# Performance work log

Hardware: AMD Instinct MI355X
Metric: run time of the kernel (lower is better)

The kernel has to match this reference:

```python
import jax, jax.numpy as jnp
import numpy as np

B, S = 4, 512
D_IN, D_H = 1600, 1600
HEADS = 50
PH = D_H // HEADS  # 32, per-head size
N_REL = 100


def setup_inputs() -> dict:
    key = jax.random.key(0)
    ks = jax.random.split(key, 14)
    w = lambda k, shape: (jax.random.normal(k, shape, jnp.float32) * 0.02)
    return {
        "hidden": jax.random.normal(ks[0], (B, S, D_IN), jnp.float32),
        "Wq": w(ks[1], (D_IN, D_H)), "bq": jnp.zeros((D_H,), jnp.float32),
        "Wk": w(ks[2], (D_IN, D_H)), "bk": jnp.zeros((D_H,), jnp.float32),
        "Wv": w(ks[3], (D_IN, D_H)), "bv": jnp.zeros((D_H,), jnp.float32),
        "Wo": w(ks[4], (D_H, D_H)), "bo": jnp.zeros((D_H,), jnp.float32),
        "rel_k_emb": w(ks[5], (N_REL, PH)),
        "rel_v_emb": w(ks[6], (N_REL, PH)),
        "W1": w(ks[7], (D_H, D_H)), "b1": jnp.zeros((D_H,), jnp.float32),
        "W2": w(ks[8], (D_H, D_H)), "b2": jnp.zeros((D_H,), jnp.float32),
        "relationship_matrix": jax.random.randint(ks[9], (B, S, S), 0, N_REL),
    }


def reference(hidden, Wq, bq, Wk, bk, Wv, bv, Wo, bo,
              rel_k_emb, rel_v_emb, W1, b1, W2, b2, relationship_matrix):
    b, s, _ = hidden.shape

    def split_heads(x):  # [b,s,D_H] -> [b,h,s,ph]
        return x.reshape(b, s, HEADS, PH).transpose(0, 2, 1, 3)

    q = split_heads(hidden @ Wq + bq)
    k = split_heads(hidden @ Wk + bk)
    v = split_heads(hidden @ Wv + bv)

    # relation-aware bias: gather per-(query,key) relation embeddings
    rel_k = rel_k_emb[relationship_matrix]  # [b,s,s,ph]
    rel_v = rel_v_emb[relationship_matrix]  # [b,s,s,ph]

    scores = jnp.einsum('bhqd,bhkd->bhqk', q, k) \
           + jnp.einsum('bhqd,bqkd->bhqk', q, rel_k)
    probs = jax.nn.softmax(scores / np.float32(np.sqrt(PH)), axis=-1)

    ctx = jnp.einsum('bhqk,bhkd->bhqd', probs, v) \
        + jnp.einsum('bhqk,bqkd->bhqd', probs, rel_v)
    ctx = ctx.transpose(0, 2, 1, 3).reshape(b, s, D_H)
    attn_out = ctx @ Wo + bo

    # position-wise FFN (hidden -> hidden -> hidden), exact gelu
    h = jax.nn.gelu(attn_out @ W1 + b1, approximate=False)
    return h @ W2 + b2
```

## Files before the change

### kernel.cpp

```cpp
#include <hip/hip_runtime.h>
#include <math.h>

#define B_   4
#define S_   512
#define DH   1600
#define NH   50
#define PH   32
#define NREL 100
#define MROWS (B_ * S_)

typedef _Float16 f16x8 __attribute__((ext_vector_type(8)));
typedef float  floatx4 __attribute__((ext_vector_type(4)));

__device__ __forceinline__ float gelu_f(float x) {
    return 0.5f * x * (1.0f + erff(x * 0.70710678118654752f));
}

__device__ __forceinline__ unsigned short f2h_u(float f) {
    _Float16 h = (_Float16)f;
    return __builtin_bit_cast(unsigned short, h);
}

typedef const __attribute__((address_space(1))) unsigned int guint;
typedef __attribute__((address_space(3))) unsigned int luint;
__device__ __forceinline__ void gl_lds16(const unsigned short* g, unsigned short* l)
{
    __builtin_amdgcn_global_load_lds((guint*)g, (luint*)l, 16, 0, 0);
}

__device__ __forceinline__ void xcd_swizzle(int& bx, int& by)
{
    const int nx = gridDim.x, nwg = nx * gridDim.y;
    const int lin = blockIdx.y * nx + blockIdx.x;
    const int cpx = nwg >> 3;
    const int swz = (lin & 7) * cpx + (lin >> 3);
    bx = swz % nx; by = swz / nx;
}

__global__ __launch_bounds__(256)
void fcast_k(const float* __restrict__ in, unsigned short* __restrict__ out, int n4)
{
    int i = blockIdx.x * 256 + threadIdx.x;
    if (i < n4) {
        float4 v = *(const float4*)&in[i * 4];
        ushort4 o = { f2h_u(v.x), f2h_u(v.y), f2h_u(v.z), f2h_u(v.w) };
        *(ushort4*)&out[i * 4] = o;
    }
}

__global__ __launch_bounds__(256)
void wcast_k(const float* __restrict__ W0, const float* __restrict__ W1,
             const float* __restrict__ W2, const float* __restrict__ W3,
             const float* __restrict__ W4, const float* __restrict__ W5,
             unsigned short* __restrict__ T)
{
    const int z = blockIdx.z;
    const float* W = (z==0)?W0:(z==1)?W1:(z==2)?W2:(z==3)?W3:(z==4)?W4:W5;
    unsigned short* out = T + (size_t)z * DH * DH;

    __shared__ float tile[32][33];
    const int t = threadIdx.x;
    const int n0 = blockIdx.x * 32, k0 = blockIdx.y * 32;
    const int r = t >> 3, c4 = (t & 7) * 4;

    float4 v = *(const float4*)&W[(size_t)(k0 + r) * DH + n0 + c4];
    tile[r][c4 + 0] = v.x; tile[r][c4 + 1] = v.y;
    tile[r][c4 + 2] = v.z; tile[r][c4 + 3] = v.w;
    __syncthreads();

    ushort4 o = { f2h_u(tile[c4 + 0][r]), f2h_u(tile[c4 + 1][r]),
                  f2h_u(tile[c4 + 2][r]), f2h_u(tile[c4 + 3][r]) };
    *(ushort4*)&out[(size_t)(n0 + r) * DH + k0 + c4] = o;
}

#define BM 128
#define BN 64
#define BK 64

template<bool GELU, bool WF32, bool WF16>
__global__ __launch_bounds__(256)
void gemm_f16_k(const unsigned short* __restrict__ Ab,
                const unsigned short* __restrict__ Bt0,
                const unsigned short* __restrict__ Bt1,
                const unsigned short* __restrict__ Bt2,
                const float* __restrict__ bi0, const float* __restrict__ bi1,
                const float* __restrict__ bi2,
                float* __restrict__ Cf0, float* __restrict__ Cf1, float* __restrict__ Cf2,
                unsigned short* __restrict__ Ch0, unsigned short* __restrict__ Ch1,
                unsigned short* __restrict__ Ch2)
{
    const int z = blockIdx.z;
    const unsigned short* Bt = (z==0)?Bt0:(z==1)?Bt1:Bt2;
    const float* bi = (z==0)?bi0:(z==1)?bi1:bi2;
    float* Cf = (z==0)?Cf0:(z==1)?Cf1:Cf2;
    unsigned short* Ch = (z==0)?Ch0:(z==1)?Ch1:Ch2;

    __shared__ __align__(16) unsigned short As[BM * BK];
    __shared__ __align__(16) unsigned short Bs[BN * BK];

    const int tid = threadIdx.x;
    const int lane = tid & 63, w = tid >> 6;
    int bx, by; xcd_swizzle(bx, by);
    const int bm = by * BM, bn = bx * BN;
    const int wm = (w >> 1) * 64, wn = (w & 1) * 32;

    const int lr8 = lane >> 3;
    const int sgrp = ((lane & 7) ^ lr8) * 8;

    const int fl_m = lane & 15, quad = lane >> 4;
    const int rs = fl_m & 7;
    const int g0 = (quad ^ rs) * 8;

    floatx4 acc[4][2] = {};

    for (int k0 = 0; k0 < DH; k0 += BK) {
        __syncthreads();
        #pragma unroll
        for (int c = 0; c < 4; c++) {
            int rowb = (c * 4 + w) * 8;
            gl_lds16(&Ab[(size_t)(bm + rowb + lr8) * DH + k0 + sgrp],
                     &As[(c * 4 + w) * 512]);
        }
        #pragma unroll
        for (int c = 0; c < 2; c++) {
            int rowb = (c * 4 + w) * 8;
            gl_lds16(&Bt[(size_t)(bn + rowb + lr8) * DH + k0 + sgrp],
                     &Bs[(c * 4 + w) * 512]);
        }
        __syncthreads();

        f16x8 af[2][4], bf[2][2];
        #pragma unroll
        for (int kk = 0; kk < 2; kk++) {
            const int gg = g0 ^ (kk * 32);
            #pragma unroll
            for (int mt = 0; mt < 4; mt++)
                af[kk][mt] = *(const f16x8*)&As[(wm + mt * 16 + fl_m) * 64 + gg];
            #pragma unroll
            for (int nt = 0; nt < 2; nt++)
                bf[kk][nt] = *(const f16x8*)&Bs[(wn + nt * 16 + fl_m) * 64 + gg];
        }

        #pragma unroll
        for (int kk = 0; kk < 2; kk++)
            #pragma unroll
            for (int mt = 0; mt < 4; mt++)
                #pragma unroll
                for (int nt = 0; nt < 2; nt++)
                    acc[mt][nt] = __builtin_amdgcn_mfma_f32_16x16x32_f16(
                        af[kk][mt], bf[kk][nt], acc[mt][nt], 0, 0, 0);
    }

    const int row_q = (lane >> 4) * 4;
    #pragma unroll
    for (int mt = 0; mt < 4; mt++) {
        #pragma unroll
        for (int nt = 0; nt < 2; nt++) {
            const int col = bn + wn + nt * 16 + fl_m;
            const float bias = bi[col];
            #pragma unroll
            for (int r = 0; r < 4; r++) {
                const int row = bm + wm + mt * 16 + row_q + r;
                float v = acc[mt][nt][r] + bias;
                if (GELU) v = gelu_f(v);
                if (WF32) Cf[(size_t)row * DH + col] = v;
                if (WF16) Ch[(size_t)row * DH + col] = f2h_u(v);
            }
        }
    }
}

__global__ __launch_bounds__(256)
void gemm_qkv3_k(const unsigned short* __restrict__ Ab,
                 const unsigned short* __restrict__ Bq,
                 const unsigned short* __restrict__ Bk,
                 const unsigned short* __restrict__ Bv,
                 const float* __restrict__ bq, const float* __restrict__ bk,
                 const float* __restrict__ bv,
                 unsigned short* __restrict__ Cq, unsigned short* __restrict__ Ck,
                 unsigned short* __restrict__ Cv)
{
    __shared__ __align__(16) unsigned short As[BM * BK];
    __shared__ __align__(16) unsigned short Bs[3][BN * BK];

    const int tid = threadIdx.x;
    const int lane = tid & 63, w = tid >> 6;
    int bx, by; xcd_swizzle(bx, by);
    const int bm = by * BM, bn = bx * BN;
    const int wm = (w >> 1) * 64, wn = (w & 1) * 32;

    const int lr8 = lane >> 3;
    const int sgrp = ((lane & 7) ^ lr8) * 8;

    const int fl_m = lane & 15, quad = lane >> 4;
    const int rs = fl_m & 7;
    const int g0 = (quad ^ rs) * 8;

    floatx4 acc[3][4][2] = {};

    for (int k0 = 0; k0 < DH; k0 += BK) {
        __syncthreads();
        #pragma unroll
        for (int c = 0; c < 4; c++) {
            int rowb = (c * 4 + w) * 8;
            gl_lds16(&Ab[(size_t)(bm + rowb + lr8) * DH + k0 + sgrp],
                     &As[(c * 4 + w) * 512]);
        }
        #pragma unroll
        for (int c = 0; c < 2; c++) {
            int rowb = (c * 4 + w) * 8;
            const size_t src = (size_t)(bn + rowb + lr8) * DH + k0 + sgrp;
            gl_lds16(&Bq[src], &Bs[0][(c * 4 + w) * 512]);
            gl_lds16(&Bk[src], &Bs[1][(c * 4 + w) * 512]);
            gl_lds16(&Bv[src], &Bs[2][(c * 4 + w) * 512]);
        }
        __syncthreads();

        #pragma unroll
        for (int kk = 0; kk < 2; kk++) {
            const int gg = g0 ^ (kk * 32);
            f16x8 af[4];
            #pragma unroll
            for (int mt = 0; mt < 4; mt++)
                af[mt] = *(const f16x8*)&As[(wm + mt * 16 + fl_m) * 64 + gg];
            #pragma unroll
            for (int z = 0; z < 3; z++) {
                f16x8 bf[2];
                #pragma unroll
                for (int nt = 0; nt < 2; nt++)
                    bf[nt] = *(const f16x8*)&Bs[z][(wn + nt * 16 + fl_m) * 64 + gg];
                #pragma unroll
                for (int mt = 0; mt < 4; mt++)
                    #pragma unroll
                    for (int nt = 0; nt < 2; nt++)
                        acc[z][mt][nt] = __builtin_amdgcn_mfma_f32_16x16x32_f16(
                            af[mt], bf[nt], acc[z][mt][nt], 0, 0, 0);
            }
        }
    }

    const int row_q = (lane >> 4) * 4;
    #pragma unroll
    for (int z = 0; z < 3; z++) {
        const float* bi = (z==0)?bq:(z==1)?bk:bv;
        unsigned short* Ch = (z==0)?Cq:(z==1)?Ck:Cv;
        #pragma unroll
        for (int mt = 0; mt < 4; mt++) {
            #pragma unroll
            for (int nt = 0; nt < 2; nt++) {
                const int col = bn + wn + nt * 16 + fl_m;
                const float bias = bi[col];
                #pragma unroll
                for (int r = 0; r < 4; r++) {
                    const int row = bm + wm + mt * 16 + row_q + r;
                    Ch[(size_t)row * DH + col] = f2h_u(acc[z][mt][nt][r] + bias);
                }
            }
        }
    }
}

__global__ __launch_bounds__(256, 1)
void attn_k(const unsigned short* __restrict__ Qg,
            const unsigned short* __restrict__ Kg,
            const unsigned short* __restrict__ Vg,
            const float* __restrict__ relk, const float* __restrict__ relv,
            const int* __restrict__ RM, unsigned short* __restrict__ CTX)
{
    __shared__ union {
        unsigned short Kb[512 * 40];
        unsigned short VT[32 * 520];
        float          qf[64 * 36];
    } big;
    __shared__ unsigned char rmb[64 * 516];
    __shared__ float qrel[64 * 101];
    __shared__ float wsum[64 * 101];
    __shared__ float relb[NREL * 36];
    __shared__ unsigned short Pb[4][2][16 * 40];

    const int tid = threadIdx.x;
    const int w = tid >> 6, lane = tid & 63;
    const int cl = lane & 15, quad = lane >> 4;
    const int b = blockIdx.z, h = blockIdx.y, q0 = blockIdx.x * 64;
    const float scale = 0.17677669529663689f;

    for (int i = tid; i < 64 * 101; i += 256) wsum[i] = 0.f;
    {
        int row = tid >> 2, g = tid & 3;
        uint4 qv = *(const uint4*)&Qg[(size_t)(b * S_ + q0 + row) * DH + h * PH + g * 8];
        f16x8 qh = __builtin_bit_cast(f16x8, qv);
        #pragma unroll
        for (int j = 0; j < 8; j++) big.qf[row * 36 + g * 8 + j] = (float)qh[j];
    }
    for (int i = tid; i < NREL * 8; i += 256) {
        int r = i >> 3, dg = i & 7;
        *(float4*)&relb[r * 36 + dg * 4] = *(const float4*)&relk[r * PH + dg * 4];
    }
    #pragma unroll
    for (int it = 0; it < 32; it++) {
        int idx = it * 256 + tid;
        int key4 = idx & 127, ql = idx >> 7;
        int4 rv = *(const int4*)&RM[(size_t)(b * S_ + q0 + ql) * S_ + key4 * 4];
        uchar4 o = { (unsigned char)rv.x, (unsigned char)rv.y,
                     (unsigned char)rv.z, (unsigned char)rv.w };
        *(uchar4*)&rmb[ql * 516 + key4 * 4] = o;
    }
    __syncthreads();

    {
        const int q = tid >> 2, rsub = tid & 3;
        float qv[PH];
        #pragma unroll
        for (int d = 0; d < PH; d++) qv[d] = big.qf[q * 36 + d];
        for (int i = 0; i < 25; i++) {
            int r = rsub * 25 + i;
            float s = 0.f;
            #pragma unroll
            for (int d = 0; d < PH; d++) s += qv[d] * relb[r * 36 + d];
            qrel[q * 101 + r] = s;
        }
    }
    __syncthreads();

    #pragma unroll
    for (int it = 0; it < 8; it++) {
        int idx = it * 256 + tid;
        int key = idx >> 2, g = idx & 3;
        uint4 kv = *(const uint4*)&Kg[(size_t)(b * S_ + key) * DH + h * PH + g * 8];
        *(uint4*)&big.Kb[key * 40 + g * 8] = kv;
    }
    for (int i = tid; i < NREL * 8; i += 256) {
        int r = i >> 3, dg = i & 7;
        *(float4*)&relb[r * 36 + dg * 4] = *(const float4*)&relv[r * PH + dg * 4];
    }
    __syncthreads();

    floatx4 acc[32];
    {
        f16x8 qa = __builtin_bit_cast(f16x8, *(const uint4*)
            &Qg[(size_t)(b * S_ + q0 + w * 16 + cl) * DH + h * PH + quad * 8]);
        #pragma unroll
        for (int t = 0; t < 32; t++) {
            f16x8 kf = *(const f16x8*)&big.Kb[(t * 16 + cl) * 40 + quad * 8];
            acc[t] = __builtin_amdgcn_mfma_f32_16x16x32_f16(qa, kf, (floatx4){}, 0, 0, 0);
        }
        #pragma unroll
        for (int t = 0; t < 32; t++) {
            #pragma unroll
            for (int r = 0; r < 4; r++) {
                int ql = w * 16 + quad * 4 + r;
                int rm = rmb[ql * 516 + t * 16 + cl];
                acc[t][r] = (acc[t][r] + qrel[ql * 101 + rm]) * scale;
            }
        }
        float mx[4] = {-1e30f, -1e30f, -1e30f, -1e30f};
        #pragma unroll
        for (int t = 0; t < 32; t++)
            #pragma unroll
            for (int r = 0; r < 4; r++) mx[r] = fmaxf(mx[r], acc[t][r]);
        #pragma unroll
        for (int r = 0; r < 4; r++) {
            #pragma unroll
            for (int off = 1; off < 16; off <<= 1)
                mx[r] = fmaxf(mx[r], __shfl_xor(mx[r], off));
        }
        float sm[4] = {};
        #pragma unroll
        for (int t = 0; t < 32; t++)
            #pragma unroll
            for (int r = 0; r < 4; r++) {
                float e = __expf(acc[t][r] - mx[r]);
                acc[t][r] = e; sm[r] += e;
            }
        #pragma unroll
        for (int r = 0; r < 4; r++) {
            #pragma unroll
            for (int off = 1; off < 16; off <<= 1)
                sm[r] += __shfl_xor(sm[r], off);
            sm[r] = 1.0f / sm[r];
        }
        #pragma unroll
        for (int t = 0; t < 32; t++)
            #pragma unroll
            for (int r = 0; r < 4; r++) acc[t][r] *= sm[r];
        #pragma unroll
        for (int t = 0; t < 32; t++) {
            #pragma unroll
            for (int r = 0; r < 4; r++) {
                int ql = w * 16 + quad * 4 + r;
                int rm = rmb[ql * 516 + t * 16 + cl];
                atomicAdd(&wsum[ql * 101 + rm], acc[t][r]);
            }
        }
    }
    __syncthreads();

    #pragma unroll
    for (int it = 0; it < 8; it++) {
        int idx = it * 256 + tid;
        int key = idx >> 2, part = idx & 3;
        uint4 vv = *(const uint4*)&Vg[(size_t)(b * S_ + key) * DH + h * PH + part * 8];
        f16x8 vh = __builtin_bit_cast(f16x8, vv);
        #pragma unroll
        for (int j = 0; j < 8; j++)
            big.VT[(part * 8 + j) * 520 + key] = f2h_u((float)vh[j]) , (void)0;
    }
    __syncthreads();

    {
        floatx4 ctx[2] = {};
        #pragma unroll
        for (int c = 0; c < 16; c++) {
            #pragma unroll
            for (int tt = 0; tt < 2; tt++) {
                #pragma unroll
                for (int r = 0; r < 4; r++)
                    Pb[w][c & 1][(quad * 4 + r) * 40 + tt * 16 + cl] =
                        f2h_u(acc[c * 2 + tt][r]);
            }
            f16x8 pa = *(const f16x8*)&Pb[w][c & 1][cl * 40 + quad * 8];
            #pragma unroll
            for (int nt = 0; nt < 2; nt++) {
                f16x8 vf = *(const f16x8*)&big.VT[(nt * 16 + cl) * 520 + c * 32 + quad * 8];
                ctx[nt] = __builtin_amdgcn_mfma_f32_16x16x32_f16(pa, vf, ctx[nt], 0, 0, 0);
            }
        }
        for (int r = 0; r < NREL; r++) {
            float rv0 = relb[r * 36 + cl];
            float rv1 = relb[r * 36 + 16 + cl];
            #pragma unroll
            for (int rr = 0; rr < 4; rr++) {
                float ws = wsum[(w * 16 + quad * 4 + rr) * 101 + r];
                ctx[0][rr] += ws * rv0;
                ctx[1][rr] += ws * rv1;
            }
        }
        #pragma unroll
        for (int nt = 0; nt < 2; nt++) {
            #pragma unroll
            for (int rr = 0; rr < 4; rr++) {
                int row = b * S_ + q0 + w * 16 + quad * 4 + rr;
                int col = h * PH + nt * 16 + cl;
                CTX[(size_t)row * DH + col] = f2h_u(ctx[nt][rr]);
            }
        }
    }
}

extern "C" void kernel_launch(void* const* d_in, const int* in_sizes, int n_in,
                              void* d_out, int out_size, void* d_ws, size_t ws_size,
                              hipStream_t stream)
{
    const float* hidden = (const float*)d_in[0];
    const float* Wq = (const float*)d_in[1];  const float* bq = (const float*)d_in[2];
    const float* Wk = (const float*)d_in[3];  const float* bk = (const float*)d_in[4];
    const float* Wv = (const float*)d_in[5];  const float* bv = (const float*)d_in[6];
    const float* Wo = (const float*)d_in[7];  const float* bo = (const float*)d_in[8];
    const float* relk = (const float*)d_in[9];
    const float* relv = (const float*)d_in[10];
    const float* W1 = (const float*)d_in[11]; const float* b1 = (const float*)d_in[12];
    const float* W2 = (const float*)d_in[13]; const float* b2 = (const float*)d_in[14];
    const int*   RM = (const int*)d_in[15];
    float* out = (float*)d_out;

    const size_t SZ = (size_t)MROWS * DH;
    const size_t SZB = SZ * 2;

    char* ws = (char*)d_ws;
    unsigned short* hb   = (unsigned short*)(ws);
    unsigned short* qf   = (unsigned short*)(ws + SZB);
    unsigned short* kf   = (unsigned short*)(ws + 2*SZB);
    unsigned short* vf   = (unsigned short*)(ws + 3*SZB);
    unsigned short* ctxf = (unsigned short*)(ws + 4*SZB);
    unsigned short* aof  = (unsigned short*)(ws + 5*SZB);
    unsigned short* hff  = (unsigned short*)(ws + 6*SZB);
    unsigned short* Wt   = (unsigned short*)(ws + 7*SZB);
    const size_t WSZ = (size_t)DH * DH;
    unsigned short *Wtq = Wt,         *Wtk = Wt + WSZ,   *Wtv = Wt + 2*WSZ,
                   *Wto = Wt + 3*WSZ, *Wt1 = Wt + 4*WSZ, *Wt2 = Wt + 5*WSZ;

    fcast_k<<<dim3((SZ/4 + 255)/256), 256, 0, stream>>>(hidden, hb, (int)(SZ/4));
    wcast_k<<<dim3(DH/32, DH/32, 6), 256, 0, stream>>>(Wq, Wk, Wv, Wo, W1, W2, Wt);

    gemm_qkv3_k<<<dim3(DH/BN, MROWS/BM), 256, 0, stream>>>(
        hb, Wtq, Wtk, Wtv, bq, bk, bv, qf, kf, vf);

    attn_k<<<dim3(S_/64, NH, B_), 256, 0, stream>>>(qf, kf, vf, relk, relv, RM, ctxf);

    gemm_f16_k<false, false, true><<<dim3(DH/BN, MROWS/BM, 1), 256, 0, stream>>>(
        ctxf, Wto, Wto, Wto, bo, bo, bo,
        nullptr, nullptr, nullptr, aof, aof, aof);

    gemm_f16_k<true, false, true><<<dim3(DH/BN, MROWS/BM, 1), 256, 0, stream>>>(
        aof, Wt1, Wt1, Wt1, b1, b1, b1,
        nullptr, nullptr, nullptr, hff, hff, hff);

    gemm_f16_k<false, true, false><<<dim3(DH/BN, MROWS/BM, 1), 256, 0, stream>>>(
        hff, Wt2, Wt2, Wt2, b2, b2, b2,
        out, out, out, nullptr, nullptr, nullptr);
}
```

Measured before the change: 717.0 us.

## Double-buffer LDS tiles in GEMM kernels to overlap global loads with MFMA

Both GEMM kernels (the generic one and the fused QKV one) now keep two shared-memory stages. The next K-tile's global-to-LDS copy is issued right after the barrier, and MFMAs then run on the current stage. This is meant to hide global load latency behind matrix compute and to remove one barrier per iteration. In exchange it doubles LDS usage, notably for the QKV kernel, which may lower the number of resident blocks per CU.

New measurement: 712.1 us. Within noise of the previous version (-0.7%).

```diff
diff --git a/kernel.cpp b/kernel.cpp
--- a/kernel.cpp
+++ b/kernel.cpp
@@ -95,8 +95,8 @@
     float* Cf = (z==0)?Cf0:(z==1)?Cf1:Cf2;
     unsigned short* Ch = (z==0)?Ch0:(z==1)?Ch1:Ch2;
 
-    __shared__ __align__(16) unsigned short As[BM * BK];
-    __shared__ __align__(16) unsigned short Bs[BN * BK];
+    __shared__ __align__(16) unsigned short As[2][BM * BK];
+    __shared__ __align__(16) unsigned short Bs[2][BN * BK];
 
     const int tid = threadIdx.x;
     const int lane = tid & 63, w = tid >> 6;
@@ -113,21 +113,26 @@
 
     floatx4 acc[4][2] = {};
 
-    for (int k0 = 0; k0 < DH; k0 += BK) {
-        __syncthreads();
+    auto STAGE = [&](int buf, int k0) {
         #pragma unroll
         for (int c = 0; c < 4; c++) {
             int rowb = (c * 4 + w) * 8;
             gl_lds16(&Ab[(size_t)(bm + rowb + lr8) * DH + k0 + sgrp],
-                     &As[(c * 4 + w) * 512]);
+                     &As[buf][(c * 4 + w) * 512]);
         }
         #pragma unroll
         for (int c = 0; c < 2; c++) {
             int rowb = (c * 4 + w) * 8;
             gl_lds16(&Bt[(size_t)(bn + rowb + lr8) * DH + k0 + sgrp],
-                     &Bs[(c * 4 + w) * 512]);
-        }
+                     &Bs[buf][(c * 4 + w) * 512]);
+        }
+    };
+
+    STAGE(0, 0);
+    int cur = 0;
+    for (int k0 = 0; k0 < DH; k0 += BK) {
         __syncthreads();
+        if (k0 + BK < DH) STAGE(cur ^ 1, k0 + BK);
 
         f16x8 af[2][4], bf[2][2];
         #pragma unroll
@@ -135,10 +140,10 @@
             const int gg = g0 ^ (kk * 32);
             #pragma unroll
             for (int mt = 0; mt < 4; mt++)
-                af[kk][mt] = *(const f16x8*)&As[(wm + mt * 16 + fl_m) * 64 + gg];
+                af[kk][mt] = *(const f16x8*)&As[cur][(wm + mt * 16 + fl_m) * 64 + gg];
             #pragma unroll
             for (int nt = 0; nt < 2; nt++)
-                bf[kk][nt] = *(const f16x8*)&Bs[(wn + nt * 16 + fl_m) * 64 + gg];
+                bf[kk][nt] = *(const f16x8*)&Bs[cur][(wn + nt * 16 + fl_m) * 64 + gg];
         }
 
         #pragma unroll
@@ -149,6 +154,7 @@
                 for (int nt = 0; nt < 2; nt++)
                     acc[mt][nt] = __builtin_amdgcn_mfma_f32_16x16x32_f16(
                         af[kk][mt], bf[kk][nt], acc[mt][nt], 0, 0, 0);
+        cur ^= 1;
     }
 
     const int row_q = (lane >> 4) * 4;
@@ -180,8 +186,8 @@
                  unsigned short* __restrict__ Cq, unsigned short* __restrict__ Ck,
                  unsigned short* __restrict__ Cv)
 {
-    __shared__ __align__(16) unsigned short As[BM * BK];
-    __shared__ __align__(16) unsigned short Bs[3][BN * BK];
+    __shared__ __align__(16) unsigned short As[2][BM * BK];
+    __shared__ __align__(16) unsigned short Bs[2][3][BN * BK];
 
     const int tid = threadIdx.x;
     const int lane = tid & 63, w = tid >> 6;
@@ -198,23 +204,28 @@
 
     floatx4 acc[3][4][2] = {};
 
-    for (int k0 = 0; k0 < DH; k0 += BK) {
-        __syncthreads();
+    auto STAGE = [&](int buf, int k0) {
         #pragma unroll
         for (int c = 0; c < 4; c++) {
             int rowb = (c * 4 + w) * 8;
             gl_lds16(&Ab[(size_t)(bm + rowb + lr8) * DH + k0 + sgrp],
-                     &As[(c * 4 + w) * 512]);
+                     &As[buf][(c * 4 + w) * 512]);
         }
         #pragma unroll
         for (int c = 0; c < 2; c++) {
             int rowb = (c * 4 + w) * 8;
             const size_t src = (size_t)(bn + rowb + lr8) * DH + k0 + sgrp;
-            gl_lds16(&Bq[src], &Bs[0][(c * 4 + w) * 512]);
-            gl_lds16(&Bk[src], &Bs[1][(c * 4 + w) * 512]);
-            gl_lds16(&Bv[src], &Bs[2][(c * 4 + w) * 512]);
-        }
+            gl_lds16(&Bq[src], &Bs[buf][0][(c * 4 + w) * 512]);
+            gl_lds16(&Bk[src], &Bs[buf][1][(c * 4 + w) * 512]);
+            gl_lds16(&Bv[src], &Bs[buf][2][(c * 4 + w) * 512]);
+        }
+    };
+
+    STAGE(0, 0);
+    int cur = 0;
+    for (int k0 = 0; k0 < DH; k0 += BK) {
         __syncthreads();
+        if (k0 + BK < DH) STAGE(cur ^ 1, k0 + BK);
 
         #pragma unroll
         for (int kk = 0; kk < 2; kk++) {
@@ -222,13 +233,13 @@
             f16x8 af[4];
             #pragma unroll
             for (int mt = 0; mt < 4; mt++)
-                af[mt] = *(const f16x8*)&As[(wm + mt * 16 + fl_m) * 64 + gg];
+                af[mt] = *(const f16x8*)&As[cur][(wm + mt * 16 + fl_m) * 64 + gg];
             #pragma unroll
             for (int z = 0; z < 3; z++) {
                 f16x8 bf[2];
                 #pragma unroll
                 for (int nt = 0; nt < 2; nt++)
-                    bf[nt] = *(const f16x8*)&Bs[z][(wn + nt * 16 + fl_m) * 64 + gg];
+                    bf[nt] = *(const f16x8*)&Bs[cur][z][(wn + nt * 16 + fl_m) * 64 + gg];
                 #pragma unroll
                 for (int mt = 0; mt < 4; mt++)
                     #pragma unroll
@@ -237,6 +248,7 @@
                             af[mt], bf[nt], acc[z][mt][nt], 0, 0, 0);
             }
         }
+        cur ^= 1;
     }
 
     const int row_q = (lane >> 4) * 4;
```
